# Optimization experiments

Hardware: AMD Instinct MI355X
Metric: run time of the kernel (lower is better)

Reference implementation:

```python
import jax, jax.numpy as jnp
import numpy as np

D_MODEL = 128
N_HEADS = 8
N_POINTS = 8
MAX_RES = 10.0


def setup_inputs() -> dict:
    key = jax.random.key(0)
    ks = jax.random.split(key, 12)
    B, C, H, W = 4, D_MODEL, 128, 128
    nh, P = N_HEADS, N_POINTS
    inp = {
        'nbr_fea': jax.random.normal(ks[0], (B, C, H, W), jnp.float32),
        'ext_fea': jax.random.normal(ks[1], (B, C, H, W), jnp.float32),
        'flow': jax.random.normal(ks[2], (B, 2, H, W), jnp.float32) * 2.0,
        'W_off': jax.random.normal(ks[3], (C, nh * P * 2), jnp.float32) * 0.02,
        'b_off': jax.random.normal(ks[4], (nh * P * 2,), jnp.float32) * 0.02,
        'W_attn': jax.random.normal(ks[5], (C, nh * P), jnp.float32) * 0.02,
        'b_attn': jnp.zeros((nh * P,), jnp.float32),
        'W_val': jax.random.normal(ks[6], (C, C), jnp.float32) * (1.0 / np.sqrt(C)),
        'b_val': jnp.zeros((C,), jnp.float32),
        'W_out': jax.random.normal(ks[7], (C, C), jnp.float32) * (1.0 / np.sqrt(C)),
        'b_out': jnp.zeros((C,), jnp.float32),
    }
    return inp


def _bilinear_gather(value, loc, H, W):
    # value: (B, nh, HW, dh)  loc: (B, nh, Q, P, 2) normalized to [0,1]
    # grid_sample semantics: align_corners=False, zero padding
    B, nh, HW, dh = value.shape
    Q, P = loc.shape[2], loc.shape[3]
    x = loc[..., 0] * W - 0.5  # (B,nh,Q,P) pixel coords
    y = loc[..., 1] * H - 0.5
    x0 = jnp.floor(x)
    y0 = jnp.floor(y)
    wx = x - x0
    wy = y - y0
    out = jnp.zeros((B, nh, Q * P, dh), value.dtype)
    for dx, dy, wgt in ((0, 0, (1 - wx) * (1 - wy)), (1, 0, wx * (1 - wy)),
                        (0, 1, (1 - wx) * wy), (1, 1, wx * wy)):
        xi = x0 + dx
        yi = y0 + dy
        valid = (xi >= 0) & (xi < W) & (yi >= 0) & (yi < H)
        xi_c = jnp.clip(xi, 0, W - 1).astype(jnp.int32)
        yi_c = jnp.clip(yi, 0, H - 1).astype(jnp.int32)
        idx = (yi_c * W + xi_c).reshape(B, nh, Q * P, 1)
        g = jnp.take_along_axis(value, idx, axis=2)  # (B,nh,QP,dh)
        w_eff = (wgt * valid.astype(value.dtype)).reshape(B, nh, Q * P, 1)
        out = out + g * w_eff
    return out.reshape(B, nh, Q, P, dh)


def reference(nbr_fea, ext_fea, flow, W_off, b_off, W_attn, b_attn, W_val, b_val, W_out, b_out):
    B, C, H, W = nbr_fea.shape
    nh, P = N_HEADS, N_POINTS
    dh = C // nh
    Q = H * W
    # normalized reference points (pixel centers / extent)
    ys = (jnp.arange(H, dtype=jnp.float32) + 0.5) / H
    xs = (jnp.arange(W, dtype=jnp.float32) + 0.5) / W
    yy, xx = jnp.meshgrid(ys, xs, indexing='ij')
    ref = jnp.stack([xx, yy], -1).reshape(Q, 2)  # (Q,2)

    ext = ext_fea.transpose(0, 2, 3, 1).reshape(B, Q, C)
    # flow-guided sampling offsets (pixels), residue bounded by tanh
    off = MAX_RES * jnp.tanh(ext @ W_off + b_off)
    off = off.reshape(B, Q, nh, P, 2)
    flow_q = flow.transpose(0, 2, 3, 1).reshape(B, Q, 1, 1, 2)
    norm = jnp.array([W, H], jnp.float32)
    loc = ref[None, :, None, None, :] + (flow_q + off) / norm  # (B,Q,nh,P,2)

    attn = jax.nn.softmax((ext @ W_attn + b_attn).reshape(B, Q, nh, P), axis=-1)

    val = (nbr_fea.transpose(0, 2, 3, 1).reshape(B, Q, C) @ W_val + b_val)
    val = val.reshape(B, Q, nh, dh).transpose(0, 2, 1, 3)  # (B,nh,HW,dh)

    sampled = _bilinear_gather(val, loc.transpose(0, 2, 1, 3, 4), H, W)  # (B,nh,Q,P,dh)
    agg = jnp.einsum('bnqpd,bqnp->bqnd', sampled, attn).reshape(B, Q, C)
    out = agg @ W_out + b_out  # (B,Q,C)
    return out.reshape(B, H, W, C).transpose(0, 3, 1, 2)
```

## Files before the change

### kernel.cpp

```cpp
#include <hip/hip_runtime.h>
#include <math.h>

namespace {
constexpr int B    = 4;
constexpr int C    = 128;
constexpr int H    = 128;
constexpr int W    = 128;
constexpr int HWn  = H * W;
constexpr int NH   = 8;
constexpr int KC   = 16;
}

__device__ __forceinline__ float fast_tanh(float x) {
  float e = __expf(2.f * x);
  return 1.f - 2.f / (e + 1.f);
}

__device__ __forceinline__ unsigned f2bf(float f) {
  unsigned u = __float_as_uint(f);
  return (u + 0x7FFFu + ((u >> 16) & 1u)) >> 16;
}

__global__ __launch_bounds__(256) void val_gemm_kernel(
    const float* __restrict__ nbr, const float* __restrict__ Wv,
    const float* __restrict__ bv, unsigned short* __restrict__ val) {
  __shared__ float a_s[KC * 64];
  __shared__ float w_s[KC * 128];
  const int t  = threadIdx.x;
  const int qi = t & 63;
  const int r  = t >> 6;
  const int b  = blockIdx.x >> 8;
  const int q0 = (blockIdx.x & 255) * 64;

  const float* Ab = nbr + (size_t)b * C * HWn + q0;
  float acc[32];
#pragma unroll
  for (int j = 0; j < 32; ++j) acc[j] = bv[32 * r + j];

  for (int ck = 0; ck < C / KC; ++ck) {
    const int k0 = ck * KC;
    {
      int k = t >> 4, cq = (t & 15) * 4;
      *(float4*)&a_s[k * 64 + cq] =
          *(const float4*)(Ab + (size_t)(k0 + k) * HWn + cq);
    }
#pragma unroll
    for (int i = 0; i < 2; ++i) {
      int idx = t + 256 * i;
      int k = idx >> 5, col = (idx & 31) * 4;
      *(float4*)&w_s[k * 128 + col] =
          *(const float4*)(Wv + (size_t)(k0 + k) * 128 + col);
    }
    __syncthreads();
#pragma unroll
    for (int k = 0; k < KC; ++k) {
      float e = a_s[k * 64 + qi];
      const float4* wp = (const float4*)&w_s[k * 128 + 32 * r];
#pragma unroll
      for (int j4 = 0; j4 < 8; ++j4) {
        float4 w = wp[j4];
        acc[4 * j4 + 0] += e * w.x; acc[4 * j4 + 1] += e * w.y;
        acc[4 * j4 + 2] += e * w.z; acc[4 * j4 + 3] += e * w.w;
      }
    }
    __syncthreads();
  }

#pragma unroll
  for (int u = 0; u < 2; ++u) {
    unsigned pk[8];
#pragma unroll
    for (int i = 0; i < 8; ++i) {
      unsigned lo = f2bf(acc[u * 16 + 2 * i]);
      unsigned hi = f2bf(acc[u * 16 + 2 * i + 1]);
      pk[i] = lo | (hi << 16);
    }
    unsigned short* dst =
        val + ((size_t)(b * NH + 2 * r + u) * HWn + q0 + qi) * 16;
    ((uint4*)dst)[0] = make_uint4(pk[0], pk[1], pk[2], pk[3]);
    ((uint4*)dst)[1] = make_uint4(pk[4], pk[5], pk[6], pk[7]);
  }
}

__global__ __launch_bounds__(256) void fused_gather_kernel(
    const float* __restrict__ ext,  const float* __restrict__ flow,
    const float* __restrict__ Woff, const float* __restrict__ boff,
    const float* __restrict__ Wattn,const float* __restrict__ battn,
    const float* __restrict__ Wout, const float* __restrict__ bout,
    const unsigned short* __restrict__ val, float* __restrict__ out) {
  __shared__ float smem[10240];
  float* a_s = smem;
  float* w_s = smem + 1024;

  const int t  = threadIdx.x;
  const int qi = t & 63;
  const int r  = t >> 6;

  const int blk    = blockIdx.x;
  const int lin    = (blk & 7) * 128 + (blk >> 3);
  const int b      = lin >> 8;
  const int tile   = lin & 255;
  const int x0     = (tile & 7) * 16;
  const int y0     = (tile >> 3) * 4;
  const int xx     = qi & 15;
  const int yy     = qi >> 4;
  const int x      = x0 + xx;
  const int y      = y0 + yy;

  const float* Eb = ext + (size_t)b * C * HWn;
  float acc[48];
#pragma unroll
  for (int j = 0; j < 32; ++j) acc[j] = boff[32 * r + j];
#pragma unroll
  for (int j = 0; j < 16; ++j) acc[32 + j] = battn[16 * r + j];

  for (int ck = 0; ck < C / KC; ++ck) {
    const int k0 = ck * KC;
    {
      int k = t >> 4, sub = t & 15;
      int row = sub >> 2, c4 = (sub & 3) * 4;
      *(float4*)&a_s[k * 64 + row * 16 + c4] =
          *(const float4*)(Eb + (size_t)(k0 + k) * HWn + (y0 + row) * W + x0 + c4);
    }
#pragma unroll
    for (int i = 0; i < 3; ++i) {
      int idx = t + 256 * i;
      int k = idx / 48;
      int j = (idx % 48) * 4;
      const float* src = (j < 128)
          ? (Woff  + (size_t)(k0 + k) * 128 + j)
          : (Wattn + (size_t)(k0 + k) * 64 + (j - 128));
      *(float4*)&w_s[k * 192 + j] = *(const float4*)src;
    }
    __syncthreads();
#pragma unroll
    for (int k = 0; k < KC; ++k) {
      float e = a_s[k * 64 + qi];
      const float4* wo = (const float4*)&w_s[k * 192 + 32 * r];
#pragma unroll
      for (int j4 = 0; j4 < 8; ++j4) {
        float4 w = wo[j4];
        acc[4 * j4 + 0] += e * w.x; acc[4 * j4 + 1] += e * w.y;
        acc[4 * j4 + 2] += e * w.z; acc[4 * j4 + 3] += e * w.w;
      }
      const float4* wa = (const float4*)&w_s[k * 192 + 128 + 16 * r];
#pragma unroll
      for (int j4 = 0; j4 < 4; ++j4) {
        float4 w = wa[j4];
        acc[32 + 4 * j4 + 0] += e * w.x; acc[32 + 4 * j4 + 1] += e * w.y;
        acc[32 + 4 * j4 + 2] += e * w.z; acc[32 + 4 * j4 + 3] += e * w.w;
      }
    }
    __syncthreads();
  }

#pragma unroll
  for (int j = 0; j < 32; ++j) acc[j] = 10.f * fast_tanh(acc[j]);
#pragma unroll
  for (int u = 0; u < 2; ++u) {
    float* a = acc + 32 + 8 * u;
    float m = a[0];
#pragma unroll
    for (int p = 1; p < 8; ++p) m = fmaxf(m, a[p]);
    float s = 0.f;
#pragma unroll
    for (int p = 0; p < 8; ++p) { float ev = __expf(a[p] - m); a[p] = ev; s += ev; }
    float inv = 1.f / s;
#pragma unroll
    for (int p = 0; p < 8; ++p) a[p] *= inv;
  }

  const float xb = (float)x + flow[(size_t)b * 2 * HWn + y * W + x];
  const float yb = (float)y + flow[((size_t)b * 2 + 1) * HWn + y * W + x];

  float agg[32];
#pragma unroll
  for (int j = 0; j < 32; ++j) agg[j] = 0.f;
  const unsigned short* valb = val + (size_t)b * NH * HWn * 16;

#pragma unroll
  for (int u = 0; u < 2; ++u) {
    const unsigned short* valh = valb + (size_t)(2 * r + u) * HWn * 16;
    float* aggh = agg + 16 * u;
#pragma unroll
    for (int p = 0; p < 8; ++p) {
      float sx = xb + acc[u * 16 + 2 * p];
      float sy = yb + acc[u * 16 + 2 * p + 1];
      float x0f = floorf(sx), y0f = floorf(sy);
      float wx = sx - x0f, wy = sy - y0f;
      int ix0 = (int)x0f, iy0 = (int)y0f;
      int ix1 = ix0 + 1,  iy1 = iy0 + 1;
      float aw  = acc[32 + u * 8 + p];
      float w00 = aw * (1.f - wx) * (1.f - wy);
      float w10 = aw * wx * (1.f - wy);
      float w01 = aw * (1.f - wx) * wy;
      float w11 = aw * wx * wy;
      if ((unsigned)ix0 >= (unsigned)W) { w00 = 0.f; w01 = 0.f; }
      if ((unsigned)ix1 >= (unsigned)W) { w10 = 0.f; w11 = 0.f; }
      if ((unsigned)iy0 >= (unsigned)H) { w00 = 0.f; w10 = 0.f; }
      if ((unsigned)iy1 >= (unsigned)H) { w01 = 0.f; w11 = 0.f; }
      int x0c = min(max(ix0, 0), W - 1);
      int x1c = min(max(ix1, 0), W - 1);
      int y0c = min(max(iy0, 0), H - 1);
      int y1c = min(max(iy1, 0), H - 1);
      const unsigned short* c00 = valh + (size_t)(y0c * W + x0c) * 16;
      const unsigned short* c10 = valh + (size_t)(y0c * W + x1c) * 16;
      const unsigned short* c01 = valh + (size_t)(y1c * W + x0c) * 16;
      const unsigned short* c11 = valh + (size_t)(y1c * W + x1c) * 16;
#pragma unroll
      for (int cn = 0; cn < 4; ++cn) {
        const unsigned short* cp = (cn == 0) ? c00 : (cn == 1) ? c10
                                  : (cn == 2) ? c01 : c11;
        float wgt = (cn == 0) ? w00 : (cn == 1) ? w10 : (cn == 2) ? w01 : w11;
        uint4 ga = ((const uint4*)cp)[0];
        uint4 gb = ((const uint4*)cp)[1];
        unsigned gs[8] = {ga.x, ga.y, ga.z, ga.w, gb.x, gb.y, gb.z, gb.w};
#pragma unroll
        for (int i = 0; i < 8; ++i) {
          float lo = __uint_as_float(gs[i] << 16);
          float hi = __uint_as_float(gs[i] & 0xFFFF0000u);
          aggh[2 * i]     += wgt * lo;
          aggh[2 * i + 1] += wgt * hi;
        }
      }
    }
  }

  float* agg_s = smem;
  float* w2_s  = smem + 8192;
#pragma unroll
  for (int j = 0; j < 32; ++j) agg_s[(32 * r + j) * 64 + qi] = agg[j];

  float acc2[32];
#pragma unroll
  for (int j = 0; j < 32; ++j) acc2[j] = bout[32 * r + j];

  for (int ck = 0; ck < C / KC; ++ck) {
    const int k0 = ck * KC;
#pragma unroll
    for (int i = 0; i < 2; ++i) {
      int idx = t + 256 * i;
      int k = idx >> 5, col = (idx & 31) * 4;
      *(float4*)&w2_s[k * 128 + col] =
          *(const float4*)(Wout + (size_t)(k0 + k) * 128 + col);
    }
    __syncthreads();
#pragma unroll
    for (int k = 0; k < KC; ++k) {
      float a = agg_s[(k0 + k) * 64 + qi];
      const float4* wp = (const float4*)&w2_s[k * 128 + 32 * r];
#pragma unroll
      for (int j4 = 0; j4 < 8; ++j4) {
        float4 w = wp[j4];
        acc2[4 * j4 + 0] += a * w.x; acc2[4 * j4 + 1] += a * w.y;
        acc2[4 * j4 + 2] += a * w.z; acc2[4 * j4 + 3] += a * w.w;
      }
    }
    __syncthreads();
  }

  float* ob = out + (size_t)b * C * HWn + y * W + x;
#pragma unroll
  for (int j = 0; j < 32; ++j)
    ob[(size_t)(32 * r + j) * HWn] = acc2[j];
}

extern "C" void kernel_launch(void* const* d_in, const int* in_sizes, int n_in,
                              void* d_out, int out_size, void* d_ws, size_t ws_size,
                              hipStream_t stream) {
  const float* nbr   = (const float*)d_in[0];
  const float* extf  = (const float*)d_in[1];
  const float* flow  = (const float*)d_in[2];
  const float* Woff  = (const float*)d_in[3];
  const float* boff  = (const float*)d_in[4];
  const float* Wattn = (const float*)d_in[5];
  const float* battn = (const float*)d_in[6];
  const float* Wval  = (const float*)d_in[7];
  const float* bval  = (const float*)d_in[8];
  const float* Wout  = (const float*)d_in[9];
  const float* bout  = (const float*)d_in[10];
  float* outp = (float*)d_out;

  unsigned short* val = (unsigned short*)d_ws;

  val_gemm_kernel<<<dim3(1024), dim3(256), 0, stream>>>(nbr, Wval, bval, val);
  fused_gather_kernel<<<dim3(1024), dim3(256), 0, stream>>>(
      extf, flow, Woff, boff, Wattn, battn, Wout, bout, val, outp);
}
```

Measured before the change: 278.1 us.

## Move all three projections to bf16 MFMA with pre-transposed bf16 weights

Result: faster. 233.2 us (-16.2%).

```diff
diff --git a/kernel.cpp b/kernel.cpp
--- a/kernel.cpp
+++ b/kernel.cpp
@@ -2,163 +2,221 @@
 #include <math.h>
 
 namespace {
-constexpr int B    = 4;
-constexpr int C    = 128;
-constexpr int H    = 128;
-constexpr int W    = 128;
-constexpr int HWn  = H * W;
-constexpr int NH   = 8;
-constexpr int KC   = 16;
-}
+constexpr int B   = 4;
+constexpr int C   = 128;
+constexpr int H   = 128;
+constexpr int W   = 128;
+constexpr int HWn = H * W;
+constexpr int NH  = 8;
+}
+
+using short8 = __attribute__((ext_vector_type(8))) short;
+using f32x4  = __attribute__((ext_vector_type(4))) float;
 
 __device__ __forceinline__ float fast_tanh(float x) {
   float e = __expf(2.f * x);
   return 1.f - 2.f / (e + 1.f);
 }
-
 __device__ __forceinline__ unsigned f2bf(float f) {
   unsigned u = __float_as_uint(f);
   return (u + 0x7FFFu + ((u >> 16) & 1u)) >> 16;
 }
+__device__ __forceinline__ unsigned pack2bf(float a, float b) {
+  return f2bf(a) | (f2bf(b) << 16);
+}
+
+__global__ __launch_bounds__(256) void prep_weights_kernel(
+    const float* __restrict__ Woff, const float* __restrict__ Wattn,
+    const float* __restrict__ Wval, const float* __restrict__ Wout,
+    unsigned short* __restrict__ wcat_t, unsigned short* __restrict__ wval_t,
+    unsigned short* __restrict__ wout_t) {
+  int row = blockIdx.x * 256 + threadIdx.x;
+  if (row >= 448) return;
+  const float* src; int ldn; int col; unsigned short* dst;
+  if (row < 192) {
+    if (row < 128) { src = Woff; ldn = 128; col = row; }
+    else           { src = Wattn; ldn = 64; col = row - 128; }
+    dst = wcat_t + row * 128;
+  } else if (row < 320) {
+    src = Wval; ldn = 128; col = row - 192; dst = wval_t + (row - 192) * 128;
+  } else {
+    src = Wout; ldn = 128; col = row - 320; dst = wout_t + (row - 320) * 128;
+  }
+  for (int k0 = 0; k0 < 128; k0 += 8) {
+    unsigned pk[4];
+#pragma unroll
+    for (int j = 0; j < 4; ++j)
+      pk[j] = pack2bf(src[(k0 + 2 * j) * ldn + col],
+                      src[(k0 + 2 * j + 1) * ldn + col]);
+    *(uint4*)(dst + k0) = make_uint4(pk[0], pk[1], pk[2], pk[3]);
+  }
+}
 
 __global__ __launch_bounds__(256) void val_gemm_kernel(
-    const float* __restrict__ nbr, const float* __restrict__ Wv,
+    const float* __restrict__ nbr, const unsigned short* __restrict__ wval_t,
     const float* __restrict__ bv, unsigned short* __restrict__ val) {
-  __shared__ float a_s[KC * 64];
-  __shared__ float w_s[KC * 128];
-  const int t  = threadIdx.x;
-  const int qi = t & 63;
-  const int r  = t >> 6;
-  const int b  = blockIdx.x >> 8;
-  const int q0 = (blockIdx.x & 255) * 64;
+  __shared__ unsigned short a_s[64 * 152];
+  __shared__ unsigned short b_s[128 * 40];
+  const int t    = threadIdx.x;
+  const int b    = blockIdx.x >> 8;
+  const int q0   = (blockIdx.x & 255) * 64;
+  const int wv   = t >> 6;
+  const int lane = t & 63;
+  const int li   = lane & 15, quad = lane >> 4;
 
   const float* Ab = nbr + (size_t)b * C * HWn + q0;
-  float acc[32];
-#pragma unroll
-  for (int j = 0; j < 32; ++j) acc[j] = bv[32 * r + j];
-
-  for (int ck = 0; ck < C / KC; ++ck) {
-    const int k0 = ck * KC;
+#pragma unroll
+  for (int it = 0; it < 4; ++it) {
+    int idx = t + 256 * it;
+    int kp  = idx >> 4;
+    int q4  = (idx & 15) * 4;
+    float4 fa = *(const float4*)(Ab + (size_t)(2 * kp) * HWn + q4);
+    float4 fb = *(const float4*)(Ab + (size_t)(2 * kp + 1) * HWn + q4);
+    const float* pa = &fa.x; const float* pb = &fb.x;
+#pragma unroll
+    for (int j = 0; j < 4; ++j)
+      *(unsigned*)&a_s[(q4 + j) * 152 + 2 * kp] = pack2bf(pa[j], pb[j]);
+  }
+
+  f32x4 acc[8];
+#pragma unroll
+  for (int n = 0; n < 8; ++n) acc[n] = (f32x4){0.f, 0.f, 0.f, 0.f};
+
+  for (int ck = 0; ck < 4; ++ck) {
+    __syncthreads();
+#pragma unroll
+    for (int it = 0; it < 2; ++it) {
+      int idx = t + 256 * it;
+      int n = idx >> 2, seg = idx & 3;
+      *(uint4*)&b_s[n * 40 + seg * 8] =
+          *(const uint4*)(wval_t + n * 128 + ck * 32 + seg * 8);
+    }
+    __syncthreads();
+    short8 af = *(const short8*)&a_s[(16 * wv + li) * 152 + ck * 32 + quad * 8];
+#pragma unroll
+    for (int n = 0; n < 8; ++n) {
+      short8 bfr = *(const short8*)&b_s[(16 * n + li) * 40 + quad * 8];
+      acc[n] = __builtin_amdgcn_mfma_f32_16x16x32_bf16(af, bfr, acc[n], 0, 0, 0);
+    }
+  }
+
+  __syncthreads();
+#pragma unroll
+  for (int n = 0; n < 8; ++n) {
+    float bias = bv[16 * n + li];
+#pragma unroll
+    for (int reg = 0; reg < 4; ++reg) {
+      int q = 16 * wv + 4 * quad + reg;
+      a_s[q * 152 + 16 * n + li] = (unsigned short)f2bf(acc[n][reg] + bias);
+    }
+  }
+  __syncthreads();
+  {
+    const int qi = t & 63, r = t >> 6;
+    uint4 v0 = *(const uint4*)&a_s[qi * 152 + 32 * r];
+    uint4 v1 = *(const uint4*)&a_s[qi * 152 + 32 * r + 8];
+    uint4 v2 = *(const uint4*)&a_s[qi * 152 + 32 * r + 16];
+    uint4 v3 = *(const uint4*)&a_s[qi * 152 + 32 * r + 24];
+    unsigned short* d0 = val + ((size_t)(b * NH + 2 * r) * HWn + q0 + qi) * 16;
+    unsigned short* d1 = val + ((size_t)(b * NH + 2 * r + 1) * HWn + q0 + qi) * 16;
+    *(uint4*)d0 = v0; *(uint4*)(d0 + 8) = v1;
+    *(uint4*)d1 = v2; *(uint4*)(d1 + 8) = v3;
+  }
+}
+
+__global__ __launch_bounds__(256) void fused_kernel(
+    const float* __restrict__ ext,  const float* __restrict__ flow,
+    const unsigned short* __restrict__ wcat_t,
+    const float* __restrict__ boff, const float* __restrict__ battn,
+    const unsigned short* __restrict__ wout_t,
+    const float* __restrict__ bout,
+    const unsigned short* __restrict__ val, float* __restrict__ out) {
+  __shared__ float smem[12352];
+  const int t    = threadIdx.x;
+  const int wv   = t >> 6;
+  const int lane = t & 63;
+  const int li   = lane & 15, quad = lane >> 4;
+  const int qi   = t & 63;
+  const int r    = t >> 6;
+
+  const int blk  = blockIdx.x;
+  const int lin  = (blk & 7) * 128 + (blk >> 3);
+  const int b    = lin >> 8;
+  const int tile = lin & 255;
+  const int x0   = (tile & 7) * 16;
+  const int y0   = (tile >> 3) * 4;
+  const int x    = x0 + (qi & 15);
+  const int y    = y0 + (qi >> 4);
+
+  unsigned short* a_s  = (unsigned short*)smem;
+  unsigned short* bw_s = (unsigned short*)(smem + 2560);
+  f32x4 acc[12];
+#pragma unroll
+  for (int n = 0; n < 12; ++n) acc[n] = (f32x4){0.f, 0.f, 0.f, 0.f};
+
+  const float* Eb = ext + (size_t)b * C * HWn;
+  for (int ck = 0; ck < 4; ++ck) {
+    const int k0 = ck * 32;
+    __syncthreads();
     {
-      int k = t >> 4, cq = (t & 15) * 4;
-      *(float4*)&a_s[k * 64 + cq] =
-          *(const float4*)(Ab + (size_t)(k0 + k) * HWn + cq);
-    }
-#pragma unroll
-    for (int i = 0; i < 2; ++i) {
-      int idx = t + 256 * i;
-      int k = idx >> 5, col = (idx & 31) * 4;
-      *(float4*)&w_s[k * 128 + col] =
-          *(const float4*)(Wv + (size_t)(k0 + k) * 128 + col);
-    }
-    __syncthreads();
-#pragma unroll
-    for (int k = 0; k < KC; ++k) {
-      float e = a_s[k * 64 + qi];
-      const float4* wp = (const float4*)&w_s[k * 128 + 32 * r];
-#pragma unroll
-      for (int j4 = 0; j4 < 8; ++j4) {
-        float4 w = wp[j4];
-        acc[4 * j4 + 0] += e * w.x; acc[4 * j4 + 1] += e * w.y;
-        acc[4 * j4 + 2] += e * w.z; acc[4 * j4 + 3] += e * w.w;
+      int kp = t >> 4;
+      int q4 = (t & 15) * 4;
+      int yy = q4 >> 4, xx = q4 & 15;
+      const float* srcp = Eb + (size_t)(k0 + 2 * kp) * HWn + (y0 + yy) * W + x0 + xx;
+      float4 fa = *(const float4*)(srcp);
+      float4 fb = *(const float4*)(srcp + HWn);
+      const float* pa = &fa.x; const float* pb = &fb.x;
+#pragma unroll
+      for (int j = 0; j < 4; ++j) {
+        unsigned ha = f2bf(pa[j]);
+        unsigned hb = f2bf(pb[j]);
+        float la = pa[j] - __uint_as_float(ha << 16);
+        float lb = pb[j] - __uint_as_float(hb << 16);
+        *(unsigned*)&a_s[(q4 + j) * 40 + 2 * kp]        = ha | (hb << 16);
+        *(unsigned*)&a_s[2560 + (q4 + j) * 40 + 2 * kp] = pack2bf(la, lb);
       }
     }
-    __syncthreads();
-  }
-
+#pragma unroll
+    for (int it = 0; it < 3; ++it) {
+      int idx = t + 256 * it;
+      int n = idx >> 2, seg = idx & 3;
+      *(uint4*)&bw_s[n * 40 + seg * 8] =
+          *(const uint4*)(wcat_t + n * 128 + k0 + seg * 8);
+    }
+    __syncthreads();
+    short8 ah = *(const short8*)&a_s[(16 * wv + li) * 40 + quad * 8];
+    short8 al = *(const short8*)&a_s[2560 + (16 * wv + li) * 40 + quad * 8];
+#pragma unroll
+    for (int n = 0; n < 12; ++n) {
+      short8 bfr = *(const short8*)&bw_s[(16 * n + li) * 40 + quad * 8];
+      acc[n] = __builtin_amdgcn_mfma_f32_16x16x32_bf16(ah, bfr, acc[n], 0, 0, 0);
+      acc[n] = __builtin_amdgcn_mfma_f32_16x16x32_bf16(al, bfr, acc[n], 0, 0, 0);
+    }
+  }
+
+  __syncthreads();
+#pragma unroll
+  for (int n = 0; n < 12; ++n) {
+    int col = 16 * n + li;
+    float bias = (col < 128) ? boff[col] : battn[col - 128];
+#pragma unroll
+    for (int reg = 0; reg < 4; ++reg) {
+      int q = 16 * wv + 4 * quad + reg;
+      smem[q * 193 + col] = acc[n][reg] + bias;
+    }
+  }
+  __syncthreads();
+
+  float offa[32];
+  float atta[16];
+#pragma unroll
+  for (int j = 0; j < 32; ++j)
+    offa[j] = 10.f * fast_tanh(smem[qi * 193 + 32 * r + j]);
+#pragma unroll
+  for (int j = 0; j < 16; ++j) atta[j] = smem[qi * 193 + 128 + 16 * r + j];
 #pragma unroll
   for (int u = 0; u < 2; ++u) {
-    unsigned pk[8];
-#pragma unroll
-    for (int i = 0; i < 8; ++i) {
-      unsigned lo = f2bf(acc[u * 16 + 2 * i]);
-      unsigned hi = f2bf(acc[u * 16 + 2 * i + 1]);
-      pk[i] = lo | (hi << 16);
-    }
-    unsigned short* dst =
-        val + ((size_t)(b * NH + 2 * r + u) * HWn + q0 + qi) * 16;
-    ((uint4*)dst)[0] = make_uint4(pk[0], pk[1], pk[2], pk[3]);
-    ((uint4*)dst)[1] = make_uint4(pk[4], pk[5], pk[6], pk[7]);
-  }
-}
-
-__global__ __launch_bounds__(256) void fused_gather_kernel(
-    const float* __restrict__ ext,  const float* __restrict__ flow,
-    const float* __restrict__ Woff, const float* __restrict__ boff,
-    const float* __restrict__ Wattn,const float* __restrict__ battn,
-    const float* __restrict__ Wout, const float* __restrict__ bout,
-    const unsigned short* __restrict__ val, float* __restrict__ out) {
-  __shared__ float smem[10240];
-  float* a_s = smem;
-  float* w_s = smem + 1024;
-
-  const int t  = threadIdx.x;
-  const int qi = t & 63;
-  const int r  = t >> 6;
-
-  const int blk    = blockIdx.x;
-  const int lin    = (blk & 7) * 128 + (blk >> 3);
-  const int b      = lin >> 8;
-  const int tile   = lin & 255;
-  const int x0     = (tile & 7) * 16;
-  const int y0     = (tile >> 3) * 4;
-  const int xx     = qi & 15;
-  const int yy     = qi >> 4;
-  const int x      = x0 + xx;
-  const int y      = y0 + yy;
-
-  const float* Eb = ext + (size_t)b * C * HWn;
-  float acc[48];
-#pragma unroll
-  for (int j = 0; j < 32; ++j) acc[j] = boff[32 * r + j];
-#pragma unroll
-  for (int j = 0; j < 16; ++j) acc[32 + j] = battn[16 * r + j];
-
-  for (int ck = 0; ck < C / KC; ++ck) {
-    const int k0 = ck * KC;
-    {
-      int k = t >> 4, sub = t & 15;
-      int row = sub >> 2, c4 = (sub & 3) * 4;
-      *(float4*)&a_s[k * 64 + row * 16 + c4] =
-          *(const float4*)(Eb + (size_t)(k0 + k) * HWn + (y0 + row) * W + x0 + c4);
-    }
-#pragma unroll
-    for (int i = 0; i < 3; ++i) {
-      int idx = t + 256 * i;
-      int k = idx / 48;
-      int j = (idx % 48) * 4;
-      const float* src = (j < 128)
-          ? (Woff  + (size_t)(k0 + k) * 128 + j)
-          : (Wattn + (size_t)(k0 + k) * 64 + (j - 128));
-      *(float4*)&w_s[k * 192 + j] = *(const float4*)src;
-    }
-    __syncthreads();
-#pragma unroll
-    for (int k = 0; k < KC; ++k) {
-      float e = a_s[k * 64 + qi];
-      const float4* wo = (const float4*)&w_s[k * 192 + 32 * r];
-#pragma unroll
-      for (int j4 = 0; j4 < 8; ++j4) {
-        float4 w = wo[j4];
-        acc[4 * j4 + 0] += e * w.x; acc[4 * j4 + 1] += e * w.y;
-        acc[4 * j4 + 2] += e * w.z; acc[4 * j4 + 3] += e * w.w;
-      }
-      const float4* wa = (const float4*)&w_s[k * 192 + 128 + 16 * r];
-#pragma unroll
-      for (int j4 = 0; j4 < 4; ++j4) {
-        float4 w = wa[j4];
-        acc[32 + 4 * j4 + 0] += e * w.x; acc[32 + 4 * j4 + 1] += e * w.y;
-        acc[32 + 4 * j4 + 2] += e * w.z; acc[32 + 4 * j4 + 3] += e * w.w;
-      }
-    }
-    __syncthreads();
-  }
-
-#pragma unroll
-  for (int j = 0; j < 32; ++j) acc[j] = 10.f * fast_tanh(acc[j]);
-#pragma unroll
-  for (int u = 0; u < 2; ++u) {
-    float* a = acc + 32 + 8 * u;
+    float* a = atta + 8 * u;
     float m = a[0];
 #pragma unroll
     for (int p = 1; p < 8; ++p) m = fmaxf(m, a[p]);
@@ -184,13 +242,13 @@
     float* aggh = agg + 16 * u;
 #pragma unroll
     for (int p = 0; p < 8; ++p) {
-      float sx = xb + acc[u * 16 + 2 * p];
-      float sy = yb + acc[u * 16 + 2 * p + 1];
+      float sx = xb + offa[u * 16 + 2 * p];
+      float sy = yb + offa[u * 16 + 2 * p + 1];
       float x0f = floorf(sx), y0f = floorf(sy);
       float wx = sx - x0f, wy = sy - y0f;
       int ix0 = (int)x0f, iy0 = (int)y0f;
       int ix1 = ix0 + 1,  iy1 = iy0 + 1;
-      float aw  = acc[32 + u * 8 + p];
+      float aw  = atta[u * 8 + p];
       float w00 = aw * (1.f - wx) * (1.f - wy);
       float w10 = aw * wx * (1.f - wy);
       float w01 = aw * (1.f - wx) * wy;
@@ -226,43 +284,55 @@
     }
   }
 
-  float* agg_s = smem;
-  float* w2_s  = smem + 8192;
-#pragma unroll
-  for (int j = 0; j < 32; ++j) agg_s[(32 * r + j) * 64 + qi] = agg[j];
-
-  float acc2[32];
-#pragma unroll
-  for (int j = 0; j < 32; ++j) acc2[j] = bout[32 * r + j];
-
-  for (int ck = 0; ck < C / KC; ++ck) {
-    const int k0 = ck * KC;
-#pragma unroll
-    for (int i = 0; i < 2; ++i) {
-      int idx = t + 256 * i;
-      int k = idx >> 5, col = (idx & 31) * 4;
-      *(float4*)&w2_s[k * 128 + col] =
-          *(const float4*)(Wout + (size_t)(k0 + k) * 128 + col);
-    }
-    __syncthreads();
-#pragma unroll
-    for (int k = 0; k < KC; ++k) {
-      float a = agg_s[(k0 + k) * 64 + qi];
-      const float4* wp = (const float4*)&w2_s[k * 128 + 32 * r];
-#pragma unroll
-      for (int j4 = 0; j4 < 8; ++j4) {
-        float4 w = wp[j4];
-        acc2[4 * j4 + 0] += a * w.x; acc2[4 * j4 + 1] += a * w.y;
-        acc2[4 * j4 + 2] += a * w.z; acc2[4 * j4 + 3] += a * w.w;
-      }
-    }
-    __syncthreads();
-  }
-
+  __syncthreads();
+  unsigned short* ag   = (unsigned short*)smem;
+  unsigned short* w2_s = (unsigned short*)(smem + 4864);
+  {
+    unsigned pk[16];
+#pragma unroll
+    for (int i = 0; i < 16; ++i) pk[i] = pack2bf(agg[2 * i], agg[2 * i + 1]);
+    uint4* dst = (uint4*)&ag[qi * 152 + 32 * r];
+    dst[0] = make_uint4(pk[0],  pk[1],  pk[2],  pk[3]);
+    dst[1] = make_uint4(pk[4],  pk[5],  pk[6],  pk[7]);
+    dst[2] = make_uint4(pk[8],  pk[9],  pk[10], pk[11]);
+    dst[3] = make_uint4(pk[12], pk[13], pk[14], pk[15]);
+  }
+
+  f32x4 acc2[8];
+#pragma unroll
+  for (int n = 0; n < 8; ++n) acc2[n] = (f32x4){0.f, 0.f, 0.f, 0.f};
+
+  for (int ck = 0; ck < 4; ++ck) {
+    __syncthreads();
+#pragma unroll
+    for (int it = 0; it < 2; ++it) {
+      int idx = t + 256 * it;
+      int n = idx >> 2, seg = idx & 3;
+      *(uint4*)&w2_s[n * 40 + seg * 8] =
+          *(const uint4*)(wout_t + n * 128 + ck * 32 + seg * 8);
+    }
+    __syncthreads();
+    short8 af = *(const short8*)&ag[(16 * wv + li) * 152 + ck * 32 + quad * 8];
+#pragma unroll
+    for (int n = 0; n < 8; ++n) {
+      short8 bfr = *(const short8*)&w2_s[(16 * n + li) * 40 + quad * 8];
+      acc2[n] = __builtin_amdgcn_mfma_f32_16x16x32_bf16(af, bfr, acc2[n], 0, 0, 0);
+    }
+  }
+
+  __syncthreads();
+#pragma unroll
+  for (int n = 0; n < 8; ++n) {
+    float bias = bout[16 * n + li];
+#pragma unroll
+    for (int reg = 0; reg < 4; ++reg)
+      smem[(16 * n + li) * 67 + 16 * wv + 4 * quad + reg] = acc2[n][reg] + bias;
+  }
+  __syncthreads();
   float* ob = out + (size_t)b * C * HWn + y * W + x;
 #pragma unroll
   for (int j = 0; j < 32; ++j)
-    ob[(size_t)(32 * r + j) * HWn] = acc2[j];
+    ob[(size_t)(32 * r + j) * HWn] = smem[(32 * r + j) * 67 + qi];
 }
 
 extern "C" void kernel_launch(void* const* d_in, const int* in_sizes, int n_in,
@@ -281,9 +351,15 @@
   const float* bout  = (const float*)d_in[10];
   float* outp = (float*)d_out;
 
-  unsigned short* val = (unsigned short*)d_ws;
-
-  val_gemm_kernel<<<dim3(1024), dim3(256), 0, stream>>>(nbr, Wval, bval, val);
-  fused_gather_kernel<<<dim3(1024), dim3(256), 0, stream>>>(
-      extf, flow, Woff, boff, Wattn, battn, Wout, bout, val, outp);
-}
+  unsigned short* val    = (unsigned short*)d_ws;
+  unsigned short* wcat_t = val + (size_t)B * NH * HWn * 16;
+  unsigned short* wval_t = wcat_t + 192 * 128;
+  unsigned short* wout_t = wval_t + 128 * 128;
+
+  prep_weights_kernel<<<dim3(2), dim3(256), 0, stream>>>(
+      Woff, Wattn, Wval, Wout, wcat_t, wval_t, wout_t);
+  val_gemm_kernel<<<dim3(1024), dim3(256), 0, stream>>>(
+      nbr, wval_t, bval, val);
+  fused_kernel<<<dim3(1024), dim3(256), 0, stream>>>(
+      extf, flow, wcat_t, boff, battn, wout_t, bout, val, outp);
+}
```
